# Kernel tuning notes

Hardware: AMD Instinct MI355X
Metric: run time of the kernel (lower is better)

## Reference

```python
import jax, jax.numpy as jnp
import numpy as np

K_SIZE = 5  # kernel_size


def _patches(f, k):
    # f: (b, c, h, w) -> (b, c, k*k, h, w), matching torch.nn.Unfold ordering
    # (patch positions row-major (kh, kw) per channel), padding = k//2, stride 1.
    p = k // 2
    b, c, h, w = f.shape
    fp = jnp.pad(f, ((0, 0), (0, 0), (p, p), (p, p)))
    slices = [fp[:, :, i:i + h, j:j + w] for i in range(k) for j in range(k)]
    return jnp.stack(slices, axis=2)


def _conv1x1(w, b, f):
    # w: (out, in), b: (out,), f: (b, in, h, w)
    return jnp.einsum('oc,bchw->bohw', w, f) + b[None, :, None, None]


def setup_inputs() -> dict:
    key = jax.random.key(0)
    ks = jax.random.split(key, 8)
    B, XC, YC, FT, H, W = 4, 64, 64, 64, 128, 128
    x = jax.random.normal(ks[0], (B, XC, H, W), dtype=jnp.float32)
    y = jax.random.normal(ks[1], (B, YC, H, W), dtype=jnp.float32)
    sx = 1.0 / np.sqrt(XC)
    sy = 1.0 / np.sqrt(YC)
    sf = 1.0 / np.sqrt(FT)
    wx = jax.random.uniform(ks[2], (FT, XC), jnp.float32, -sx, sx)
    bx = jax.random.uniform(ks[3], (FT,), jnp.float32, -sx, sx)
    wy = jax.random.uniform(ks[4], (FT, YC), jnp.float32, -sy, sy)
    by = jax.random.uniform(ks[5], (FT,), jnp.float32, -sy, sy)
    wo = jax.random.uniform(ks[6], (XC, FT), jnp.float32, -sf, sf)
    bo = jax.random.uniform(ks[7], (XC,), jnp.float32, -sf, sf)
    return {"x": x, "y": y, "wx": wx, "bx": bx, "wy": wy, "by": by, "wo": wo, "bo": bo}


def reference(x, y, wx, bx, wy, by, wo, bo):
    k = K_SIZE
    q = _conv1x1(wy, by, y)            # (b, feat, h, w): Q (the q axis of size 1 is squeezed)
    Kp = _patches(q, k)                # (b, feat, k^2, h, w): unfold(conv_y(y))
    v = _conv1x1(wx, bx, x)            # (b, feat, h, w)
    Vp = _patches(v, k)                # (b, feat, k^2, h, w): unfold(conv_x(x))
    A = jnp.einsum('bckhw,bchw->bkhw', Kp, q)   # scores over k^2 neighbors
    A = jax.nn.softmax(A, axis=1)               # softmax over dim=1 (k^2)
    out = jnp.einsum('bkhw,bckhw->bchw', A, Vp)  # aggregate values
    out = _conv1x1(wo, bo, out)
    return out + x
```

## Files before the change

kernel.cpp:

```cpp
#include <hip/hip_runtime.h>

#define HH   128
#define WW   128
#define HW   (HH * WW)
#define CC   64
#define TILE 16
#define HALO 20
#define NHP  (HALO * HALO)
#define SWZ(r) (((r) >> 1) & 7)

typedef unsigned int uint32;
typedef _Float16 h2   __attribute__((ext_vector_type(2)));
typedef __fp16   h2b  __attribute__((ext_vector_type(2)));
typedef _Float16 h8   __attribute__((ext_vector_type(8)));
typedef float    f32x4 __attribute__((ext_vector_type(4)));

__device__ __forceinline__ uint32 pkrtz(float a, float b) {
    h2b r = __builtin_amdgcn_cvt_pkrtz(a, b);
    return __builtin_bit_cast(uint32, r);
}
__device__ __forceinline__ float dot2(uint32 a, uint32 b, float c) {
#if __has_builtin(__builtin_amdgcn_fdot2)
    return __builtin_amdgcn_fdot2(__builtin_bit_cast(h2b, a),
                                  __builtin_bit_cast(h2b, b), c, false);
#else
    h2 x = __builtin_bit_cast(h2, a), y = __builtin_bit_cast(h2, b);
    return c + (float)x.x * (float)y.x + (float)x.y * (float)y.y;
#endif
}
__device__ __forceinline__ f32x4 mfma16(uint4 a, uint4 b, f32x4 c) {
    return __builtin_amdgcn_mfma_f32_16x16x32_f16(
        __builtin_bit_cast(h8, a), __builtin_bit_cast(h8, b), c, 0, 0, 0);
}
__device__ __forceinline__ uint4 pack_w8(const float* __restrict__ w) {
    const float4 lo = *(const float4*)w;
    const float4 hi = *(const float4*)(w + 4);
    uint4 r;
    r.x = pkrtz(lo.x, lo.y); r.y = pkrtz(lo.z, lo.w);
    r.z = pkrtz(hi.x, hi.y); r.w = pkrtz(hi.z, hi.w);
    return r;
}

__global__ __launch_bounds__(1024, 4)
void fused_attn(const float* __restrict__ x, const float* __restrict__ y,
                const float* __restrict__ wx, const float* __restrict__ bx,
                const float* __restrict__ wy, const float* __restrict__ by,
                const float* __restrict__ wo, const float* __restrict__ bo,
                float* __restrict__ out)
{
    __shared__ uint32 Ah[NHP * 32];
    __shared__ uint32 Bh[NHP * 32];

    const int lin  = blockIdx.x;
    const int xcd  = lin & 7;
    const int rr   = lin >> 3;
    const int b    = xcd >> 1;
    const int half = xcd & 1;
    const int ty0  = ((rr >> 3) + half * 4) * TILE;
    const int tx0  = (rr & 7) * TILE;

    const int t = threadIdx.x;

    for (int i = t; i < NHP * 8 / 2; i += 1024) {
        const int c   = i / 200;
        const int rem = i - c * 200;
        const int hy  = rem / 10;
        const int hx  = (rem - hy * 10) * 2;
        const int pix = hy * HALO + hx;
        int gy = ty0 + hy - 2, gx = tx0 + hx - 2;
        const bool ok = ((unsigned)gy < HH) & ((unsigned)gx < (WW - 1));
        if (!ok) { gy = 0; gx = 0; }
        const size_t base = (size_t)b * CC * HW + (size_t)(c * 8) * HW
                          + (size_t)gy * WW + gx;
        float2 yv[8], xv[8];
        #pragma unroll
        for (int j = 0; j < 8; ++j) {
            yv[j] = *(const float2*)(y + base + (size_t)j * HW);
            xv[j] = *(const float2*)(x + base + (size_t)j * HW);
        }
        uint4 q0, q1;
        q0.x = pkrtz(yv[0].x, yv[1].x); q0.y = pkrtz(yv[2].x, yv[3].x);
        q0.z = pkrtz(yv[4].x, yv[5].x); q0.w = pkrtz(yv[6].x, yv[7].x);
        q1.x = pkrtz(yv[0].y, yv[1].y); q1.y = pkrtz(yv[2].y, yv[3].y);
        q1.z = pkrtz(yv[4].y, yv[5].y); q1.w = pkrtz(yv[6].y, yv[7].y);
        *(uint4*)&Ah[pix * 32 + (c ^ SWZ(pix)) * 4]           = q0;
        *(uint4*)&Ah[(pix + 1) * 32 + (c ^ SWZ(pix + 1)) * 4] = q1;
        q0.x = pkrtz(xv[0].x, xv[1].x); q0.y = pkrtz(xv[2].x, xv[3].x);
        q0.z = pkrtz(xv[4].x, xv[5].x); q0.w = pkrtz(xv[6].x, xv[7].x);
        q1.x = pkrtz(xv[0].y, xv[1].y); q1.y = pkrtz(xv[2].y, xv[3].y);
        q1.z = pkrtz(xv[4].y, xv[5].y); q1.w = pkrtz(xv[6].y, xv[7].y);
        *(uint4*)&Bh[pix * 32 + (c ^ SWZ(pix)) * 4]           = q0;
        *(uint4*)&Bh[(pix + 1) * 32 + (c ^ SWZ(pix + 1)) * 4] = q1;
    }
    __syncthreads();

    const int wv = t >> 6;
    const int ln = t & 63;
    const int lm = ln & 15;
    const int qd = ln >> 4;
    const int ot = wv & 3;

    f32x4 accq[7], accv[7];
    uint2 xres[4];
    {
        const uint4 aq0 = pack_w8(wy + (ot * 16 + lm) * CC + qd * 8);
        const uint4 aq1 = pack_w8(wy + (ot * 16 + lm) * CC + qd * 8 + 32);
        const uint4 av0 = pack_w8(wx + (ot * 16 + lm) * CC + qd * 8);
        const uint4 av1 = pack_w8(wx + (ot * 16 + lm) * CC + qd * 8 + 32);
        #pragma unroll
        for (int k = 0; k < 7; ++k) {
            const int j = wv + k * 16;
            if (j < 100) {
                const int px = (j >> 2) * 16 + lm, sw = SWZ(px);
                const uint4 b0 = *(const uint4*)&Ah[px * 32 + ((qd    ) ^ sw) * 4];
                const uint4 b1 = *(const uint4*)&Ah[px * 32 + ((qd + 4) ^ sw) * 4];
                f32x4 a = {0.f, 0.f, 0.f, 0.f};
                a = mfma16(aq0, b0, a); a = mfma16(aq1, b1, a); accq[k] = a;
                const uint4 c0 = *(const uint4*)&Bh[px * 32 + ((qd    ) ^ sw) * 4];
                const uint4 c1 = *(const uint4*)&Bh[px * 32 + ((qd + 4) ^ sw) * 4];
                f32x4 v = {0.f, 0.f, 0.f, 0.f};
                v = mfma16(av0, c0, v); v = mfma16(av1, c1, v); accv[k] = v;
            }
        }
        #pragma unroll
        for (int k = 0; k < 4; ++k) {
            const int px = ((wv >> 2) + k * 4) * 16 + lm;
            const int hpix = ((px >> 4) + 2) * HALO + (px & 15) + 2;
            const int chunk = ot * 2 + (qd >> 1);
            xres[k] = *(const uint2*)
                &Bh[hpix * 32 + (chunk ^ SWZ(hpix)) * 4 + (qd & 1) * 2];
        }
    }
    __syncthreads();

    {
        const float4 bq = *(const float4*)(by + ot * 16 + qd * 4);
        const float4 bv = *(const float4*)(bx + ot * 16 + qd * 4);
        const int chunk = ot * 2 + (qd >> 1);
        #pragma unroll
        for (int k = 0; k < 7; ++k) {
            const int j = wv + k * 16;
            if (j < 100) {
                const int px = (j >> 2) * 16 + lm;
                const int hy = px / HALO, hx = px - hy * HALO;
                const int gy = ty0 + hy - 2, gx = tx0 + hx - 2;
                uint2 wq = {0u, 0u}, wvv = {0u, 0u};
                if (((unsigned)gy < HH) & ((unsigned)gx < WW)) {
                    wq.x  = pkrtz(accq[k].x + bq.x, accq[k].y + bq.y);
                    wq.y  = pkrtz(accq[k].z + bq.z, accq[k].w + bq.w);
                    wvv.x = pkrtz(accv[k].x + bv.x, accv[k].y + bv.y);
                    wvv.y = pkrtz(accv[k].z + bv.z, accv[k].w + bv.w);
                }
                const int off = px * 32 + (chunk ^ SWZ(px)) * 4 + (qd & 1) * 2;
                *(uint2*)&Ah[off] = wq;
                *(uint2*)&Bh[off] = wvv;
            }
        }
    }
    __syncthreads();

    const int p    = t >> 2, sub = t & 3;
    const int py   = p >> 4, pxl = p & 15;
    const int crow = (py + 2) * HALO + (pxl + 2);

    uint32 qc[8];
    {
        const int c0 = ((2 * sub)     ^ SWZ(crow)) * 4;
        const int c1 = ((2 * sub + 1) ^ SWZ(crow)) * 4;
        *(uint4*)&qc[0] = *(const uint4*)&Ah[crow * 32 + c0];
        *(uint4*)&qc[4] = *(const uint4*)&Ah[crow * 32 + c1];
    }

    float sc[25];
    #pragma unroll
    for (int dy = 0; dy < 5; ++dy)
        #pragma unroll
        for (int dx = 0; dx < 5; ++dx) {
            const int nrow = (py + dy) * HALO + (pxl + dx);
            const int c0 = ((2 * sub)     ^ SWZ(nrow)) * 4;
            const int c1 = ((2 * sub + 1) ^ SWZ(nrow)) * 4;
            const uint4 r0 = *(const uint4*)&Ah[nrow * 32 + c0];
            const uint4 r1 = *(const uint4*)&Ah[nrow * 32 + c1];
            float s = 0.f;
            s = dot2(qc[0], r0.x, s); s = dot2(qc[1], r0.y, s);
            s = dot2(qc[2], r0.z, s); s = dot2(qc[3], r0.w, s);
            s = dot2(qc[4], r1.x, s); s = dot2(qc[5], r1.y, s);
            s = dot2(qc[6], r1.z, s); s = dot2(qc[7], r1.w, s);
            s += __shfl_xor(s, 1);
            s += __shfl_xor(s, 2);
            sc[dy * 5 + dx] = s;
        }

    float mx = sc[0];
    #pragma unroll
    for (int k = 1; k < 25; ++k) mx = fmaxf(mx, sc[k]);
    float sum = 0.f;
    #pragma unroll
    for (int k = 0; k < 25; ++k) { sc[k] = __expf(sc[k] - mx); sum += sc[k]; }
    const float inv = 1.f / sum;

    h2 ag[8];
    #pragma unroll
    for (int k = 0; k < 8; ++k) ag[k] = (h2)(_Float16)0;
    #pragma unroll
    for (int dy = 0; dy < 5; ++dy)
        #pragma unroll
        for (int dx = 0; dx < 5; ++dx) {
            const int nrow = (py + dy) * HALO + (pxl + dx);
            const int c0 = ((2 * sub)     ^ SWZ(nrow)) * 4;
            const int c1 = ((2 * sub + 1) ^ SWZ(nrow)) * 4;
            const uint4 r0 = *(const uint4*)&Bh[nrow * 32 + c0];
            const uint4 r1 = *(const uint4*)&Bh[nrow * 32 + c1];
            const _Float16 af = (_Float16)(sc[dy * 5 + dx] * inv);
            const h2 a2 = {af, af};
            ag[0] += a2 * __builtin_bit_cast(h2, r0.x);
            ag[1] += a2 * __builtin_bit_cast(h2, r0.y);
            ag[2] += a2 * __builtin_bit_cast(h2, r0.z);
            ag[3] += a2 * __builtin_bit_cast(h2, r0.w);
            ag[4] += a2 * __builtin_bit_cast(h2, r1.x);
            ag[5] += a2 * __builtin_bit_cast(h2, r1.y);
            ag[6] += a2 * __builtin_bit_cast(h2, r1.z);
            ag[7] += a2 * __builtin_bit_cast(h2, r1.w);
        }

    __syncthreads();
    {
        const int c0 = ((2 * sub)     ^ SWZ(p)) * 4;
        const int c1 = ((2 * sub + 1) ^ SWZ(p)) * 4;
        uint4 w0, w1;
        w0.x = __builtin_bit_cast(uint32, ag[0]); w0.y = __builtin_bit_cast(uint32, ag[1]);
        w0.z = __builtin_bit_cast(uint32, ag[2]); w0.w = __builtin_bit_cast(uint32, ag[3]);
        w1.x = __builtin_bit_cast(uint32, ag[4]); w1.y = __builtin_bit_cast(uint32, ag[5]);
        w1.z = __builtin_bit_cast(uint32, ag[6]); w1.w = __builtin_bit_cast(uint32, ag[7]);
        *(uint4*)&Ah[p * 32 + c0] = w0;
        *(uint4*)&Ah[p * 32 + c1] = w1;
    }
    __syncthreads();

    {
        const uint4 a0 = pack_w8(wo + (ot * 16 + lm) * CC + qd * 8);
        const uint4 a1 = pack_w8(wo + (ot * 16 + lm) * CC + qd * 8 + 32);
        const float4 bq = *(const float4*)(bo + ot * 16 + qd * 4);
        #pragma unroll
        for (int k = 0; k < 4; ++k) {
            const int px = ((wv >> 2) + k * 4) * 16 + lm, sw = SWZ(px);
            const uint4 b0 = *(const uint4*)&Ah[px * 32 + ((qd    ) ^ sw) * 4];
            const uint4 b1 = *(const uint4*)&Ah[px * 32 + ((qd + 4) ^ sw) * 4];
            f32x4 a = {0.f, 0.f, 0.f, 0.f};
            a = mfma16(a0, b0, a);
            a = mfma16(a1, b1, a);
            const int gh = ty0 + (px >> 4), gw = tx0 + (px & 15);
            const h2 xp0 = __builtin_bit_cast(h2, xres[k].x);
            const h2 xp1 = __builtin_bit_cast(h2, xres[k].y);
            const float rv[4] = {(float)xp0.x, (float)xp0.y,
                                 (float)xp1.x, (float)xp1.y};
            const float av4[4] = {a.x + bq.x, a.y + bq.y, a.z + bq.z, a.w + bq.w};
            #pragma unroll
            for (int r = 0; r < 4; ++r) {
                const int oc = ot * 16 + qd * 4 + r;
                const size_t ad = (size_t)(b * CC + oc) * HW + (size_t)gh * WW + gw;
                out[ad] = av4[r] + rv[r];
            }
        }
    }
}

extern "C" void kernel_launch(void* const* d_in, const int* in_sizes, int n_in,
                              void* d_out, int out_size, void* d_ws, size_t ws_size,
                              hipStream_t stream) {
    const float* x  = (const float*)d_in[0];
    const float* y  = (const float*)d_in[1];
    const float* wx = (const float*)d_in[2];
    const float* bx = (const float*)d_in[3];
    const float* wy = (const float*)d_in[4];
    const float* by = (const float*)d_in[5];
    const float* wo = (const float*)d_in[6];
    const float* bo = (const float*)d_in[7];
    float* out = (float*)d_out;
    (void)d_ws; (void)ws_size;

    fused_attn<<<dim3(256), 1024, 0, stream>>>(x, y, wx, bx, wy, by, wo, bo, out);
}
```

Before: 114.5 us.

## Stage Q and V projections separately so V conversion overlaps Q work

```diff
diff --git a/kernel.cpp b/kernel.cpp
--- a/kernel.cpp
+++ b/kernel.cpp
@@ -61,36 +61,59 @@
 
     const int t = threadIdx.x;
 
-    for (int i = t; i < NHP * 8 / 2; i += 1024) {
-        const int c   = i / 200;
-        const int rem = i - c * 200;
-        const int hy  = rem / 10;
-        const int hx  = (rem - hy * 10) * 2;
-        const int pix = hy * HALO + hx;
+    float2 yv0[8], xv0[8], yv1[8], xv1[8];
+    int pix0 = 0, co0 = 0, pix1 = 0, co1 = 0;
+    const bool has1 = t < (NHP * 8 / 2 - 1024);
+    {
+        const int i = t;
+        co0 = i / 200;
+        const int rem = i - co0 * 200;
+        const int hy = rem / 10, hx = (rem - hy * 10) * 2;
+        pix0 = hy * HALO + hx;
         int gy = ty0 + hy - 2, gx = tx0 + hx - 2;
         const bool ok = ((unsigned)gy < HH) & ((unsigned)gx < (WW - 1));
         if (!ok) { gy = 0; gx = 0; }
-        const size_t base = (size_t)b * CC * HW + (size_t)(c * 8) * HW
+        const size_t base = (size_t)b * CC * HW + (size_t)(co0 * 8) * HW
                           + (size_t)gy * WW + gx;
-        float2 yv[8], xv[8];
         #pragma unroll
         for (int j = 0; j < 8; ++j) {
-            yv[j] = *(const float2*)(y + base + (size_t)j * HW);
-            xv[j] = *(const float2*)(x + base + (size_t)j * HW);
-        }
+            yv0[j] = *(const float2*)(y + base + (size_t)j * HW);
+            xv0[j] = *(const float2*)(x + base + (size_t)j * HW);
+        }
+    }
+    if (has1) {
+        const int i = t + 1024;
+        co1 = i / 200;
+        const int rem = i - co1 * 200;
+        const int hy = rem / 10, hx = (rem - hy * 10) * 2;
+        pix1 = hy * HALO + hx;
+        int gy = ty0 + hy - 2, gx = tx0 + hx - 2;
+        const bool ok = ((unsigned)gy < HH) & ((unsigned)gx < (WW - 1));
+        if (!ok) { gy = 0; gx = 0; }
+        const size_t base = (size_t)b * CC * HW + (size_t)(co1 * 8) * HW
+                          + (size_t)gy * WW + gx;
+        #pragma unroll
+        for (int j = 0; j < 8; ++j) {
+            yv1[j] = *(const float2*)(y + base + (size_t)j * HW);
+            xv1[j] = *(const float2*)(x + base + (size_t)j * HW);
+        }
+    }
+    {
         uint4 q0, q1;
-        q0.x = pkrtz(yv[0].x, yv[1].x); q0.y = pkrtz(yv[2].x, yv[3].x);
-        q0.z = pkrtz(yv[4].x, yv[5].x); q0.w = pkrtz(yv[6].x, yv[7].x);
-        q1.x = pkrtz(yv[0].y, yv[1].y); q1.y = pkrtz(yv[2].y, yv[3].y);
-        q1.z = pkrtz(yv[4].y, yv[5].y); q1.w = pkrtz(yv[6].y, yv[7].y);
-        *(uint4*)&Ah[pix * 32 + (c ^ SWZ(pix)) * 4]           = q0;
-        *(uint4*)&Ah[(pix + 1) * 32 + (c ^ SWZ(pix + 1)) * 4] = q1;
-        q0.x = pkrtz(xv[0].x, xv[1].x); q0.y = pkrtz(xv[2].x, xv[3].x);
-        q0.z = pkrtz(xv[4].x, xv[5].x); q0.w = pkrtz(xv[6].x, xv[7].x);
-        q1.x = pkrtz(xv[0].y, xv[1].y); q1.y = pkrtz(xv[2].y, xv[3].y);
-        q1.z = pkrtz(xv[4].y, xv[5].y); q1.w = pkrtz(xv[6].y, xv[7].y);
-        *(uint4*)&Bh[pix * 32 + (c ^ SWZ(pix)) * 4]           = q0;
-        *(uint4*)&Bh[(pix + 1) * 32 + (c ^ SWZ(pix + 1)) * 4] = q1;
+        q0.x = pkrtz(yv0[0].x, yv0[1].x); q0.y = pkrtz(yv0[2].x, yv0[3].x);
+        q0.z = pkrtz(yv0[4].x, yv0[5].x); q0.w = pkrtz(yv0[6].x, yv0[7].x);
+        q1.x = pkrtz(yv0[0].y, yv0[1].y); q1.y = pkrtz(yv0[2].y, yv0[3].y);
+        q1.z = pkrtz(yv0[4].y, yv0[5].y); q1.w = pkrtz(yv0[6].y, yv0[7].y);
+        *(uint4*)&Ah[pix0 * 32 + (co0 ^ SWZ(pix0)) * 4]           = q0;
+        *(uint4*)&Ah[(pix0 + 1) * 32 + (co0 ^ SWZ(pix0 + 1)) * 4] = q1;
+        if (has1) {
+            q0.x = pkrtz(yv1[0].x, yv1[1].x); q0.y = pkrtz(yv1[2].x, yv1[3].x);
+            q0.z = pkrtz(yv1[4].x, yv1[5].x); q0.w = pkrtz(yv1[6].x, yv1[7].x);
+            q1.x = pkrtz(yv1[0].y, yv1[1].y); q1.y = pkrtz(yv1[2].y, yv1[3].y);
+            q1.z = pkrtz(yv1[4].y, yv1[5].y); q1.w = pkrtz(yv1[6].y, yv1[7].y);
+            *(uint4*)&Ah[pix1 * 32 + (co1 ^ SWZ(pix1)) * 4]           = q0;
+            *(uint4*)&Ah[(pix1 + 1) * 32 + (co1 ^ SWZ(pix1 + 1)) * 4] = q1;
+        }
     }
     __syncthreads();
 
@@ -100,13 +123,10 @@
     const int qd = ln >> 4;
     const int ot = wv & 3;
 
-    f32x4 accq[7], accv[7];
-    uint2 xres[4];
+    f32x4 accq[7];
     {
         const uint4 aq0 = pack_w8(wy + (ot * 16 + lm) * CC + qd * 8);
         const uint4 aq1 = pack_w8(wy + (ot * 16 + lm) * CC + qd * 8 + 32);
-        const uint4 av0 = pack_w8(wx + (ot * 16 + lm) * CC + qd * 8);
-        const uint4 av1 = pack_w8(wx + (ot * 16 + lm) * CC + qd * 8 + 32);
         #pragma unroll
         for (int k = 0; k < 7; ++k) {
             const int j = wv + k * 16;
@@ -115,27 +135,34 @@
                 const uint4 b0 = *(const uint4*)&Ah[px * 32 + ((qd    ) ^ sw) * 4];
                 const uint4 b1 = *(const uint4*)&Ah[px * 32 + ((qd + 4) ^ sw) * 4];
                 f32x4 a = {0.f, 0.f, 0.f, 0.f};
-                a = mfma16(aq0, b0, a); a = mfma16(aq1, b1, a); accq[k] = a;
-                const uint4 c0 = *(const uint4*)&Bh[px * 32 + ((qd    ) ^ sw) * 4];
-                const uint4 c1 = *(const uint4*)&Bh[px * 32 + ((qd + 4) ^ sw) * 4];
-                f32x4 v = {0.f, 0.f, 0.f, 0.f};
-                v = mfma16(av0, c0, v); v = mfma16(av1, c1, v); accv[k] = v;
-            }
-        }
-        #pragma unroll
-        for (int k = 0; k < 4; ++k) {
-            const int px = ((wv >> 2) + k * 4) * 16 + lm;
-            const int hpix = ((px >> 4) + 2) * HALO + (px & 15) + 2;
-            const int chunk = ot * 2 + (qd >> 1);
-            xres[k] = *(const uint2*)
-                &Bh[hpix * 32 + (chunk ^ SWZ(hpix)) * 4 + (qd & 1) * 2];
-        }
-    }
-    __syncthreads();
-
+                a = mfma16(aq0, b0, a); a = mfma16(aq1, b1, a);
+                accq[k] = a;
+            }
+        }
+    }
+    {
+        uint4 q0, q1;
+        q0.x = pkrtz(xv0[0].x, xv0[1].x); q0.y = pkrtz(xv0[2].x, xv0[3].x);
+        q0.z = pkrtz(xv0[4].x, xv0[5].x); q0.w = pkrtz(xv0[6].x, xv0[7].x);
+        q1.x = pkrtz(xv0[0].y, xv0[1].y); q1.y = pkrtz(xv0[2].y, xv0[3].y);
+        q1.z = pkrtz(xv0[4].y, xv0[5].y); q1.w = pkrtz(xv0[6].y, xv0[7].y);
+        *(uint4*)&Bh[pix0 * 32 + (co0 ^ SWZ(pix0)) * 4]           = q0;
+        *(uint4*)&Bh[(pix0 + 1) * 32 + (co0 ^ SWZ(pix0 + 1)) * 4] = q1;
+        if (has1) {
+            q0.x = pkrtz(xv1[0].x, xv1[1].x); q0.y = pkrtz(xv1[2].x, xv1[3].x);
+            q0.z = pkrtz(xv1[4].x, xv1[5].x); q0.w = pkrtz(xv1[6].x, xv1[7].x);
+            q1.x = pkrtz(xv1[0].y, xv1[1].y); q1.y = pkrtz(xv1[2].y, xv1[3].y);
+            q1.z = pkrtz(xv1[4].y, xv1[5].y); q1.w = pkrtz(xv1[6].y, xv1[7].y);
+            *(uint4*)&Bh[pix1 * 32 + (co1 ^ SWZ(pix1)) * 4]           = q0;
+            *(uint4*)&Bh[(pix1 + 1) * 32 + (co1 ^ SWZ(pix1 + 1)) * 4] = q1;
+        }
+    }
+    __syncthreads();
+
+    f32x4 accv[7];
+    uint2 xres[4];
     {
         const float4 bq = *(const float4*)(by + ot * 16 + qd * 4);
-        const float4 bv = *(const float4*)(bx + ot * 16 + qd * 4);
         const int chunk = ot * 2 + (qd >> 1);
         #pragma unroll
         for (int k = 0; k < 7; ++k) {
@@ -144,21 +171,57 @@
                 const int px = (j >> 2) * 16 + lm;
                 const int hy = px / HALO, hx = px - hy * HALO;
                 const int gy = ty0 + hy - 2, gx = tx0 + hx - 2;
-                uint2 wq = {0u, 0u}, wvv = {0u, 0u};
+                uint2 wq = {0u, 0u};
                 if (((unsigned)gy < HH) & ((unsigned)gx < WW)) {
-                    wq.x  = pkrtz(accq[k].x + bq.x, accq[k].y + bq.y);
-                    wq.y  = pkrtz(accq[k].z + bq.z, accq[k].w + bq.w);
+                    wq.x = pkrtz(accq[k].x + bq.x, accq[k].y + bq.y);
+                    wq.y = pkrtz(accq[k].z + bq.z, accq[k].w + bq.w);
+                }
+                *(uint2*)&Ah[px * 32 + (chunk ^ SWZ(px)) * 4 + (qd & 1) * 2] = wq;
+            }
+        }
+        const uint4 av0 = pack_w8(wx + (ot * 16 + lm) * CC + qd * 8);
+        const uint4 av1 = pack_w8(wx + (ot * 16 + lm) * CC + qd * 8 + 32);
+        #pragma unroll
+        for (int k = 0; k < 7; ++k) {
+            const int j = wv + k * 16;
+            if (j < 100) {
+                const int px = (j >> 2) * 16 + lm, sw = SWZ(px);
+                const uint4 c0 = *(const uint4*)&Bh[px * 32 + ((qd    ) ^ sw) * 4];
+                const uint4 c1 = *(const uint4*)&Bh[px * 32 + ((qd + 4) ^ sw) * 4];
+                f32x4 v = {0.f, 0.f, 0.f, 0.f};
+                v = mfma16(av0, c0, v); v = mfma16(av1, c1, v);
+                accv[k] = v;
+            }
+        }
+        #pragma unroll
+        for (int k = 0; k < 4; ++k) {
+            const int px = ((wv >> 2) + k * 4) * 16 + lm;
+            const int hpix = ((px >> 4) + 2) * HALO + (px & 15) + 2;
+            xres[k] = *(const uint2*)
+                &Bh[hpix * 32 + (chunk ^ SWZ(hpix)) * 4 + (qd & 1) * 2];
+        }
+    }
+    __syncthreads();
+
+    {
+        const float4 bv = *(const float4*)(bx + ot * 16 + qd * 4);
+        const int chunk = ot * 2 + (qd >> 1);
+        #pragma unroll
+        for (int k = 0; k < 7; ++k) {
+            const int j = wv + k * 16;
+            if (j < 100) {
+                const int px = (j >> 2) * 16 + lm;
+                const int hy = px / HALO, hx = px - hy * HALO;
+                const int gy = ty0 + hy - 2, gx = tx0 + hx - 2;
+                uint2 wvv = {0u, 0u};
+                if (((unsigned)gy < HH) & ((unsigned)gx < WW)) {
                     wvv.x = pkrtz(accv[k].x + bv.x, accv[k].y + bv.y);
                     wvv.y = pkrtz(accv[k].z + bv.z, accv[k].w + bv.w);
                 }
-                const int off = px * 32 + (chunk ^ SWZ(px)) * 4 + (qd & 1) * 2;
-                *(uint2*)&Ah[off] = wq;
-                *(uint2*)&Bh[off] = wvv;
-            }
-        }
-    }
-    __syncthreads();
-
+                *(uint2*)&Bh[px * 32 + (chunk ^ SWZ(px)) * 4 + (qd & 1) * 2] = wvv;
+            }
+        }
+    }
     const int p    = t >> 2, sub = t & 3;
     const int py   = p >> 4, pxl = p & 15;
     const int crow = (py + 2) * HALO + (pxl + 2);
@@ -191,13 +254,17 @@
             sc[dy * 5 + dx] = s;
         }
 
-    float mx = sc[0];
-    #pragma unroll
-    for (int k = 1; k < 25; ++k) mx = fmaxf(mx, sc[k]);
-    float sum = 0.f;
-    #pragma unroll
-    for (int k = 0; k < 25; ++k) { sc[k] = __expf(sc[k] - mx); sum += sc[k]; }
+    float mx = sc[24];
+    #pragma unroll
+    for (int k = 0; k < 24; k += 2) mx = fmaxf(mx, fmaxf(sc[k], sc[k + 1]));
+    #pragma unroll
+    for (int k = 0; k < 25; ++k) sc[k] = __expf(sc[k] - mx);
+    float sum = sc[24];
+    #pragma unroll
+    for (int k = 0; k < 24; k += 2) sum += sc[k] + sc[k + 1];
     const float inv = 1.f / sum;
+
+    __syncthreads();
 
     h2 ag[8];
     #pragma unroll
@@ -222,8 +289,6 @@
             ag[6] += a2 * __builtin_bit_cast(h2, r1.z);
             ag[7] += a2 * __builtin_bit_cast(h2, r1.w);
         }
-
-    __syncthreads();
     {
         const int c0 = ((2 * sub)     ^ SWZ(p)) * 4;
         const int c1 = ((2 * sub + 1) ^ SWZ(p)) * 4;
```

Result: no change. 114.6 us (+0.1%).

## Process two horizontally adjacent pixels per thread group to share neighbor LDS loads

Applied to the files above, without the earlier changes.

```diff
diff --git a/kernel.cpp b/kernel.cpp
--- a/kernel.cpp
+++ b/kernel.cpp
@@ -27,6 +27,11 @@
     h2 x = __builtin_bit_cast(h2, a), y = __builtin_bit_cast(h2, b);
     return c + (float)x.x * (float)y.x + (float)x.y * (float)y.y;
 #endif
+}
+__device__ __forceinline__ float dot16(uint4 q, uint4 r, float s) {
+    s = dot2(q.x, r.x, s); s = dot2(q.y, r.y, s);
+    s = dot2(q.z, r.z, s); s = dot2(q.w, r.w, s);
+    return s;
 }
 __device__ __forceinline__ f32x4 mfma16(uint4 a, uint4 b, f32x4 c) {
     return __builtin_amdgcn_mfma_f32_16x16x32_f16(
@@ -159,81 +164,92 @@
     }
     __syncthreads();
 
-    const int p    = t >> 2, sub = t & 3;
-    const int py   = p >> 4, pxl = p & 15;
-    const int crow = (py + 2) * HALO + (pxl + 2);
-
-    uint32 qc[8];
-    {
-        const int c0 = ((2 * sub)     ^ SWZ(crow)) * 4;
-        const int c1 = ((2 * sub + 1) ^ SWZ(crow)) * 4;
-        *(uint4*)&qc[0] = *(const uint4*)&Ah[crow * 32 + c0];
-        *(uint4*)&qc[4] = *(const uint4*)&Ah[crow * 32 + c1];
-    }
-
-    float sc[25];
+    const int g   = t >> 3, sub = t & 7;
+    const int py  = g >> 3, pc2 = (g & 7) * 2;
+    const int crA = (py + 2) * HALO + (pc2 + 2);
+    const int crB = crA + 1;
+
+    const uint4 qa = *(const uint4*)&Ah[crA * 32 + (sub ^ SWZ(crA)) * 4];
+    const uint4 qb = *(const uint4*)&Ah[crB * 32 + (sub ^ SWZ(crB)) * 4];
+
+    float sa[25], sb[25];
+    #pragma unroll
+    for (int k = 0; k < 25; ++k) { sa[k] = 0.f; sb[k] = 0.f; }
     #pragma unroll
     for (int dy = 0; dy < 5; ++dy)
         #pragma unroll
-        for (int dx = 0; dx < 5; ++dx) {
-            const int nrow = (py + dy) * HALO + (pxl + dx);
-            const int c0 = ((2 * sub)     ^ SWZ(nrow)) * 4;
-            const int c1 = ((2 * sub + 1) ^ SWZ(nrow)) * 4;
-            const uint4 r0 = *(const uint4*)&Ah[nrow * 32 + c0];
-            const uint4 r1 = *(const uint4*)&Ah[nrow * 32 + c1];
-            float s = 0.f;
-            s = dot2(qc[0], r0.x, s); s = dot2(qc[1], r0.y, s);
-            s = dot2(qc[2], r0.z, s); s = dot2(qc[3], r0.w, s);
-            s = dot2(qc[4], r1.x, s); s = dot2(qc[5], r1.y, s);
-            s = dot2(qc[6], r1.z, s); s = dot2(qc[7], r1.w, s);
-            s += __shfl_xor(s, 1);
-            s += __shfl_xor(s, 2);
-            sc[dy * 5 + dx] = s;
-        }
-
-    float mx = sc[0];
-    #pragma unroll
-    for (int k = 1; k < 25; ++k) mx = fmaxf(mx, sc[k]);
-    float sum = 0.f;
-    #pragma unroll
-    for (int k = 0; k < 25; ++k) { sc[k] = __expf(sc[k] - mx); sum += sc[k]; }
-    const float inv = 1.f / sum;
-
-    h2 ag[8];
-    #pragma unroll
-    for (int k = 0; k < 8; ++k) ag[k] = (h2)(_Float16)0;
+        for (int du = 0; du < 6; ++du) {
+            const int nrow = (py + dy) * HALO + (pc2 + du);
+            const uint4 r = *(const uint4*)&Ah[nrow * 32 + (sub ^ SWZ(nrow)) * 4];
+            if (du < 5) sa[dy * 5 + du]     = dot16(qa, r, sa[dy * 5 + du]);
+            if (du > 0) sb[dy * 5 + du - 1] = dot16(qb, r, sb[dy * 5 + du - 1]);
+        }
+    #pragma unroll
+    for (int k = 0; k < 25; ++k) {
+        float v = sa[k];
+        v += __shfl_xor(v, 1); v += __shfl_xor(v, 2); v += __shfl_xor(v, 4);
+        sa[k] = v;
+        float w = sb[k];
+        w += __shfl_xor(w, 1); w += __shfl_xor(w, 2); w += __shfl_xor(w, 4);
+        sb[k] = w;
+    }
+
+    {
+        float mxa = sa[24], mxb = sb[24];
+        #pragma unroll
+        for (int k = 0; k < 24; k += 2) {
+            mxa = fmaxf(mxa, fmaxf(sa[k], sa[k + 1]));
+            mxb = fmaxf(mxb, fmaxf(sb[k], sb[k + 1]));
+        }
+        float suma = 0.f, sumb = 0.f;
+        #pragma unroll
+        for (int k = 0; k < 25; ++k) {
+            sa[k] = __expf(sa[k] - mxa); suma += sa[k];
+            sb[k] = __expf(sb[k] - mxb); sumb += sb[k];
+        }
+        const float iva = 1.f / suma, ivb = 1.f / sumb;
+        #pragma unroll
+        for (int k = 0; k < 25; ++k) { sa[k] *= iva; sb[k] *= ivb; }
+    }
+
+    h2 aga[4], agb[4];
+    #pragma unroll
+    for (int k = 0; k < 4; ++k) { aga[k] = (h2)(_Float16)0; agb[k] = (h2)(_Float16)0; }
     #pragma unroll
     for (int dy = 0; dy < 5; ++dy)
         #pragma unroll
-        for (int dx = 0; dx < 5; ++dx) {
-            const int nrow = (py + dy) * HALO + (pxl + dx);
-            const int c0 = ((2 * sub)     ^ SWZ(nrow)) * 4;
-            const int c1 = ((2 * sub + 1) ^ SWZ(nrow)) * 4;
-            const uint4 r0 = *(const uint4*)&Bh[nrow * 32 + c0];
-            const uint4 r1 = *(const uint4*)&Bh[nrow * 32 + c1];
-            const _Float16 af = (_Float16)(sc[dy * 5 + dx] * inv);
-            const h2 a2 = {af, af};
-            ag[0] += a2 * __builtin_bit_cast(h2, r0.x);
-            ag[1] += a2 * __builtin_bit_cast(h2, r0.y);
-            ag[2] += a2 * __builtin_bit_cast(h2, r0.z);
-            ag[3] += a2 * __builtin_bit_cast(h2, r0.w);
-            ag[4] += a2 * __builtin_bit_cast(h2, r1.x);
-            ag[5] += a2 * __builtin_bit_cast(h2, r1.y);
-            ag[6] += a2 * __builtin_bit_cast(h2, r1.z);
-            ag[7] += a2 * __builtin_bit_cast(h2, r1.w);
-        }
-
-    __syncthreads();
-    {
-        const int c0 = ((2 * sub)     ^ SWZ(p)) * 4;
-        const int c1 = ((2 * sub + 1) ^ SWZ(p)) * 4;
-        uint4 w0, w1;
-        w0.x = __builtin_bit_cast(uint32, ag[0]); w0.y = __builtin_bit_cast(uint32, ag[1]);
-        w0.z = __builtin_bit_cast(uint32, ag[2]); w0.w = __builtin_bit_cast(uint32, ag[3]);
-        w1.x = __builtin_bit_cast(uint32, ag[4]); w1.y = __builtin_bit_cast(uint32, ag[5]);
-        w1.z = __builtin_bit_cast(uint32, ag[6]); w1.w = __builtin_bit_cast(uint32, ag[7]);
-        *(uint4*)&Ah[p * 32 + c0] = w0;
-        *(uint4*)&Ah[p * 32 + c1] = w1;
+        for (int du = 0; du < 6; ++du) {
+            const int nrow = (py + dy) * HALO + (pc2 + du);
+            const uint4 r = *(const uint4*)&Bh[nrow * 32 + (sub ^ SWZ(nrow)) * 4];
+            if (du < 5) {
+                const _Float16 af = (_Float16)sa[dy * 5 + du];
+                const h2 a2 = {af, af};
+                aga[0] += a2 * __builtin_bit_cast(h2, r.x);
+                aga[1] += a2 * __builtin_bit_cast(h2, r.y);
+                aga[2] += a2 * __builtin_bit_cast(h2, r.z);
+                aga[3] += a2 * __builtin_bit_cast(h2, r.w);
+            }
+            if (du > 0) {
+                const _Float16 bf = (_Float16)sb[dy * 5 + du - 1];
+                const h2 b2 = {bf, bf};
+                agb[0] += b2 * __builtin_bit_cast(h2, r.x);
+                agb[1] += b2 * __builtin_bit_cast(h2, r.y);
+                agb[2] += b2 * __builtin_bit_cast(h2, r.z);
+                agb[3] += b2 * __builtin_bit_cast(h2, r.w);
+            }
+        }
+
+    __syncthreads();
+
+    {
+        const int pa = py * 16 + pc2, pb = pa + 1;
+        uint4 wa, wb;
+        wa.x = __builtin_bit_cast(uint32, aga[0]); wa.y = __builtin_bit_cast(uint32, aga[1]);
+        wa.z = __builtin_bit_cast(uint32, aga[2]); wa.w = __builtin_bit_cast(uint32, aga[3]);
+        wb.x = __builtin_bit_cast(uint32, agb[0]); wb.y = __builtin_bit_cast(uint32, agb[1]);
+        wb.z = __builtin_bit_cast(uint32, agb[2]); wb.w = __builtin_bit_cast(uint32, agb[3]);
+        *(uint4*)&Ah[pa * 32 + (sub ^ SWZ(pa)) * 4] = wa;
+        *(uint4*)&Ah[pb * 32 + (sub ^ SWZ(pb)) * 4] = wb;
     }
     __syncthreads();
 
```

Result: slower. 126.3 us (+10.3%).
